# Kernel tuning notes

Hardware: AMD Instinct MI355X
Metric: run time of the kernel (lower is better)

## Reference

```python
import jax, jax.numpy as jnp
import numpy as np

D = 1024      # model dim
H = 16        # attention heads
E = 8         # experts
TOP_K = 2
CF = 1.25     # capacity factor
EPS = 1e-5
BAL_COEF = 1e-2
Z_COEF = 1e-3


def layer_norm(x, w, b):
    m = x.mean(-1, keepdims=True)
    var = ((x - m) ** 2).mean(-1, keepdims=True)
    return (x - m) * jax.lax.rsqrt(var + EPS) * w + b


def mha(q, k, v, in_w, in_b, out_w, out_b):
    B, S, d = q.shape
    dh = d // H
    wq, wk, wv = jnp.split(in_w, 3, axis=0)
    bq, bk, bv = jnp.split(in_b, 3)

    def proj(x, w, b):  # [B,S,d] -> [B,H,S,dh]
        return (x @ w.T + b).reshape(B, -1, H, dh).transpose(0, 2, 1, 3)

    qh, kh, vh = proj(q, wq, bq), proj(k, wk, bk), proj(v, wv, bv)
    scale = 1.0 / np.sqrt(dh)
    scores = jnp.einsum('bhqd,bhkd->bhqk', qh, kh) * scale
    attn = jax.nn.softmax(scores, axis=-1)
    o = jnp.einsum('bhqk,bhkd->bhqd', attn, vh).transpose(0, 2, 1, 3).reshape(B, S, d)
    return o @ out_w.T + out_b


def moe(x, router_w, w1, b1, w2, b2):
    B, S, d = x.shape
    t = x.reshape(-1, d)           # [N,d] tokens
    N = t.shape[0]
    C = int(np.ceil(TOP_K * N / E * CF))  # per-expert capacity (static)
    logits = t @ router_w          # [N,E]
    probs = jax.nn.softmax(logits, axis=-1)
    gates, idx = jax.lax.top_k(probs, TOP_K)   # [N,2]
    oh = jax.nn.one_hot(idx, E, dtype=t.dtype) # [N,2,E]
    m0, m1 = oh[:, 0], oh[:, 1]
    # position in expert buffer; first choices take priority over second
    pos0 = jnp.cumsum(m0, axis=0) - 1.0
    pos1 = jnp.cumsum(m1, axis=0) - 1.0 + m0.sum(axis=0, keepdims=True)
    v0 = m0 * (pos0 < C)
    v1 = m1 * (pos1 < C)
    p0 = jax.nn.one_hot(pos0.astype(jnp.int32), C, dtype=t.dtype) * v0[..., None]  # [N,E,C]
    p1 = jax.nn.one_hot(pos1.astype(jnp.int32), C, dtype=t.dtype) * v1[..., None]
    dispatch = p0 + p1
    combine = p0 * gates[:, 0, None, None] + p1 * gates[:, 1, None, None]
    # dispatch -> grouped GEMM -> combine
    xin = jnp.einsum('nec,nd->ecd', dispatch, t)                     # [E,C,d]
    h = jax.nn.gelu(jnp.einsum('ecd,edf->ecf', xin, w1) + b1[:, None, :])
    out_e = jnp.einsum('ecf,efd->ecd', h, w2) + b2[:, None, :]       # [E,C,d]
    y = jnp.einsum('nec,ecd->nd', combine, out_e).reshape(B, S, d)
    # aux losses: load-balance + router z-loss
    f = m0.mean(axis=0)            # fraction routed (top-1)
    P = probs.mean(axis=0)         # mean router prob
    balance = E * jnp.sum(f * P)
    zloss = jnp.mean(jax.nn.logsumexp(logits, axis=-1) ** 2)
    aux = BAL_COEF * balance + Z_COEF * zloss
    return y, aux


def setup_inputs() -> dict:
    key = jax.random.key(0)
    ks = jax.random.split(key, 16)
    s = 0.02
    Dff = 4 * D
    return {
        'q': jax.random.normal(ks[0], (8, 512, D), jnp.float32),
        'k': jax.random.normal(ks[1], (8, 512, D), jnp.float32),
        'v': jax.random.normal(ks[2], (8, 512, D), jnp.float32),
        'in_proj_w': jax.random.normal(ks[3], (3 * D, D), jnp.float32) * s,
        'in_proj_b': jnp.zeros((3 * D,), jnp.float32),
        'out_proj_w': jax.random.normal(ks[4], (D, D), jnp.float32) * s,
        'out_proj_b': jnp.zeros((D,), jnp.float32),
        'ln1_w': jnp.ones((D,), jnp.float32),
        'ln1_b': jnp.zeros((D,), jnp.float32),
        'ln2_w': jnp.ones((D,), jnp.float32),
        'ln2_b': jnp.zeros((D,), jnp.float32),
        'router_w': jax.random.normal(ks[5], (D, E), jnp.float32) * s,
        'w1': jax.random.normal(ks[6], (E, D, Dff), jnp.float32) * s,
        'b1': jnp.zeros((E, Dff), jnp.float32),
        'w2': jax.random.normal(ks[7], (E, Dff, D), jnp.float32) * s,
        'b2': jnp.zeros((E, D), jnp.float32),
    }


def reference(q, k, v, in_proj_w, in_proj_b, out_proj_w, out_proj_b,
              ln1_w, ln1_b, ln2_w, ln2_b, router_w, w1, b1, w2, b2):
    attn = mha(q, k, v, in_proj_w, in_proj_b, out_proj_w, out_proj_b)
    x = layer_norm(q + attn, ln1_w, ln1_b)
    y, aux = moe(x, router_w, w1, b1, w2, b2)
    x = layer_norm(x + y, ln2_w, ln2_b)
    return x, aux
```

## Files before the change

kernel.cpp:

```cpp
#include <hip/hip_runtime.h>
#include <cstdint>
#include <cstddef>

#define KB   8
#define KS   512
#define KD   1024
#define KH   16
#define KDH  64
#define KE   8
#define KDFF 4096
#define KN   4096
#define KCAP 1280
#define KCHB 32
#define KNCH 4
#define KPLE ((long)KN*KD)

typedef unsigned short u16;
typedef _Float16 f16;
typedef f16   f16x8 __attribute__((ext_vector_type(8)));
typedef float f32x4 __attribute__((ext_vector_type(4)));

#define RSCALE 4096.0f
#define RINV   2.44140625e-4f

__device__ __forceinline__ u16 f2h(float f){
  f16 h = (f16)f;
  return __builtin_bit_cast(u16, h);
}
__device__ __forceinline__ float h2f(u16 u){
  f16 h = __builtin_bit_cast(f16, u);
  return (float)h;
}
__device__ __forceinline__ void split2v(float f, u16 &a, u16 &b){
  f16 h0 = (f16)f;
  float r = (f - (float)h0) * RSCALE;
  a = __builtin_bit_cast(u16, h0);
  b = f2h(r);
}
__device__ __forceinline__ f16x8 ld8h(const u16* p){
  uint4 v = *(const uint4*)p;
  return __builtin_bit_cast(f16x8, v);
}
__device__ __forceinline__ void async16(const u16* g, u16* l){
  __builtin_amdgcn_global_load_lds(
      (const __attribute__((address_space(1))) unsigned int*)(g),
      (__attribute__((address_space(3))) unsigned int*)(l),
      16, 0, 0);
}

__device__ __forceinline__ int xcd_remap(int lin, int nwg){
  int qq = nwg >> 3, r8 = nwg & 7;
  int xcd = lin & 7, pos = lin >> 3;
  return (xcd < r8 ? xcd*(qq+1) : r8*(qq+1) + (xcd-r8)*qq) + pos;
}

struct GArgs {
  const u16 *A0, *A1;
  const u16 *B0, *B1;
  long lda, sA, ldb, sB;
  const float* bias; long biasStride;
  float* outF;
  u16 *o0;
  u16 *o1;
  int K, mode;
  int hbase;
  float scale;
};

template<int NP>
__launch_bounds__(256)
__global__ void gemm128(GArgs g){
  __shared__ __align__(16) u16 sm[NP*2*4096];
  const int tid  = threadIdx.x;
  const int lane = tid & 63;
  const int wave = tid >> 6;
  const int quad = lane >> 4;
  const int r    = lane & 15;
  const int wm = (wave & 1) * 64;
  const int wn = (wave >> 1) * 64;
  const int gx = gridDim.x, gy = gridDim.y;
  const int nwg = gx*gy*(int)gridDim.z;
  int lin = (int)blockIdx.x + gx*((int)blockIdx.y + gy*(int)blockIdx.z);
  lin = xcd_remap(lin, nwg);
  const int bx = lin % gx;
  const int byy = (lin / gx) % gy;
  const int z  = lin / (gx*gy);
  const long m0 = (long)byy * 128;
  const long n0 = (long)bx * 128;
  const u16* Ap[NP]; const u16* Bp[NP];
  if (g.mode == 2){
    int bh = g.hbase + z;
    long off = ((long)(bh >> 4)*KS)*KD + (long)(bh & 15)*KDH;
    Ap[0] = g.A0 + off; Bp[0] = g.B0 + off;
    if (NP == 2){ Ap[1] = g.A1 + off; Bp[1] = g.B1 + off; }
  } else {
    Ap[0] = g.A0 + (long)z*g.sA; Bp[0] = g.B0 + (long)z*g.sB;
    if (NP == 2){ Ap[1] = g.A1 + (long)z*g.sA; Bp[1] = g.B1 + (long)z*g.sB; }
  }
  const int srow   = tid >> 2;
  const int schunk = (tid & 3) ^ ((tid >> 3) & 3);
  f32x4 acc[4][4] = {};
  f32x4 accr[4][4] = {};
  for (int kt = 0; kt < g.K; kt += 32){
#pragma unroll
    for (int p = 0; p < NP; ++p){
#pragma unroll
      for (int r0 = 0; r0 < 2; ++r0){
        long row = r0*64 + srow;
        async16(Ap[p] + (m0 + row)*g.lda + kt + schunk*8, &sm[p*4096      + r0*2048 + wave*512]);
        async16(Bp[p] + (n0 + row)*g.ldb + kt + schunk*8, &sm[(NP+p)*4096 + r0*2048 + wave*512]);
      }
    }
    __syncthreads();
    f16x8 af[NP][4], bf[NP][4];
#pragma unroll
    for (int i = 0; i < 4; ++i){
      int row = wm + i*16 + r;
      int slot = quad ^ ((row >> 1) & 3);
#pragma unroll
      for (int p = 0; p < NP; ++p)
        af[p][i] = ld8h(&sm[p*4096 + row*32 + slot*8]);
    }
#pragma unroll
    for (int j = 0; j < 4; ++j){
      int row = wn + j*16 + r;
      int slot = quad ^ ((row >> 1) & 3);
#pragma unroll
      for (int p = 0; p < NP; ++p)
        bf[p][j] = ld8h(&sm[(NP+p)*4096 + row*32 + slot*8]);
    }
#pragma unroll
    for (int i = 0; i < 4; ++i)
#pragma unroll
      for (int j = 0; j < 4; ++j){
        acc[i][j] = __builtin_amdgcn_mfma_f32_16x16x32_f16(af[0][i], bf[0][j], acc[i][j], 0, 0, 0);
        if (NP == 2){
          accr[i][j] = __builtin_amdgcn_mfma_f32_16x16x32_f16(af[0][i], bf[1][j], accr[i][j], 0, 0, 0);
          accr[i][j] = __builtin_amdgcn_mfma_f32_16x16x32_f16(af[1][i], bf[0][j], accr[i][j], 0, 0, 0);
        }
      }
    __syncthreads();
  }
#pragma unroll
  for (int i = 0; i < 4; ++i){
#pragma unroll
    for (int rr = 0; rr < 4; ++rr){
      long row = m0 + wm + i*16 + quad*4 + rr;
#pragma unroll
      for (int j = 0; j < 4; ++j){
        long col = n0 + wn + j*16 + r;
        float v = acc[i][j][rr];
        if (NP == 2) v += accr[i][j][rr] * RINV;
        switch (g.mode){
          case 2: {
            g.outF[((long)z*KS + row)*KS + col] = v * g.scale;
            break;
          }
          case 4: {
            v += g.bias[col];
            g.outF[row*KD + col] = v;
            break;
          }
          case 5: {
            v += g.bias[(long)z*g.biasStride + col];
            float u = v + 0.044715f*v*v*v;
            v = 0.5f*v*(1.0f + tanhf(0.7978845608028654f*u));
            g.o0[((long)z*KCAP + row)*KDFF + col] = f2h(v);
            break;
          }
          case 6: {
            v += g.bias[(long)z*g.biasStride + col];
            g.o0[((long)z*KCAP + row)*KD + col] = f2h(v);
            break;
          }
          default: {
            v += g.bias[(long)z*g.biasStride + col];
            u16* d0 = (z < 2) ? (g.o0 + (long)z*2*KPLE) : g.o1;
            u16* d1 = d0 + KPLE;
            long idx = row*KD + col;
            unsigned short x, y; split2v(v, x, y);
            d0[idx] = x; d1[idx] = y;
            break;
          }
        }
      }
    }
  }
}

__launch_bounds__(256)
__global__ void gemm_pv(const u16* __restrict__ Ph, const u16* __restrict__ Pl,
                        const u16* __restrict__ V0, const u16* __restrict__ V1,
                        u16* __restrict__ O0, u16* __restrict__ O1, int chunkBase){
  __shared__ __align__(16) u16 sm[2*4096 + 2*2048];
  const int tid  = threadIdx.x;
  const int lane = tid & 63;
  const int wave = tid >> 6;
  const int quad = lane >> 4;
  const int r    = lane & 15;
  const int wm = (wave & 1) * 64;
  const int wn = (wave >> 1) * 32;
  const int gx = gridDim.x;
  const int nwg = gx*(int)gridDim.y;
  int lin = (int)blockIdx.x + gx*(int)blockIdx.y;
  lin = xcd_remap(lin, nwg);
  const int z  = lin / gx;
  const long m0 = (long)(lin % gx) * 128;
  const u16* Ap[2] = { Ph + (long)z*KS*KS,  Pl + (long)z*KS*KS };
  const u16* Bp[2] = { V0 + (long)z*KDH*KS, V1 + (long)z*KDH*KS };
  const int srow   = tid >> 2;
  const int schunk = (tid & 3) ^ ((tid >> 3) & 3);
  f32x4 acc[4][2] = {};
  f32x4 accr[4][2] = {};
  for (int kt = 0; kt < KS; kt += 32){
#pragma unroll
    for (int p = 0; p < 2; ++p){
#pragma unroll
      for (int r0 = 0; r0 < 2; ++r0){
        long row = r0*64 + srow;
        async16(Ap[p] + (m0 + row)*KS + kt + schunk*8, &sm[p*4096 + r0*2048 + wave*512]);
      }
      async16(Bp[p] + srow*KS + kt + schunk*8, &sm[8192 + p*2048 + wave*512]);
    }
    __syncthreads();
    f16x8 af[2][4], bf[2][2];
#pragma unroll
    for (int i = 0; i < 4; ++i){
      int row = wm + i*16 + r;
      int slot = quad ^ ((row >> 1) & 3);
#pragma unroll
      for (int p = 0; p < 2; ++p)
        af[p][i] = ld8h(&sm[p*4096 + row*32 + slot*8]);
    }
#pragma unroll
    for (int j = 0; j < 2; ++j){
      int row = wn + j*16 + r;
      int slot = quad ^ ((row >> 1) & 3);
#pragma unroll
      for (int p = 0; p < 2; ++p)
        bf[p][j] = ld8h(&sm[8192 + p*2048 + row*32 + slot*8]);
    }
#pragma unroll
    for (int i = 0; i < 4; ++i)
#pragma unroll
      for (int j = 0; j < 2; ++j){
        acc[i][j]  = __builtin_amdgcn_mfma_f32_16x16x32_f16(af[0][i], bf[0][j], acc[i][j], 0, 0, 0);
        accr[i][j] = __builtin_amdgcn_mfma_f32_16x16x32_f16(af[0][i], bf[1][j], accr[i][j], 0, 0, 0);
        accr[i][j] = __builtin_amdgcn_mfma_f32_16x16x32_f16(af[1][i], bf[0][j], accr[i][j], 0, 0, 0);
      }
    __syncthreads();
  }
  int bh = chunkBase + z;
  long b = bh >> 4, h = bh & 15;
#pragma unroll
  for (int i = 0; i < 4; ++i){
#pragma unroll
    for (int rr = 0; rr < 4; ++rr){
      long s = m0 + wm + i*16 + quad*4 + rr;
#pragma unroll
      for (int j = 0; j < 2; ++j){
        long col = wn + j*16 + r;
        float v = acc[i][j][rr] + accr[i][j][rr] * RINV;
        long idx = (b*KS + s)*KD + h*KDH + col;
        unsigned short x, y; split2v(v, x, y);
        O0[idx] = x; O1[idx] = y;
      }
    }
  }
}

__global__ void split2k(const float* __restrict__ x, u16* __restrict__ h,
                        u16* __restrict__ l, long n4){
  long i = (long)blockIdx.x*blockDim.x + threadIdx.x;
  if (i >= n4) return;
  float4 v = ((const float4*)x)[i];
  ushort4 a, b;
  split2v(v.x, a.x, b.x);
  split2v(v.y, a.y, b.y);
  split2v(v.z, a.z, b.z);
  split2v(v.w, a.w, b.w);
  ((ushort4*)h)[i] = a; ((ushort4*)l)[i] = b;
}

__global__ void trans_b(const float* __restrict__ in, u16* __restrict__ outp, int R, int Cc){
  __shared__ float tile[32][33];
  long z = blockIdx.z;
  const float* ip = in + z*(long)R*Cc;
  u16* op = outp + z*(long)R*Cc;
  int c0 = blockIdx.x*32, r0 = blockIdx.y*32;
  int tx = threadIdx.x, ty = threadIdx.y;
  for (int rr = ty; rr < 32; rr += 8)
    tile[rr][tx] = ip[(long)(r0+rr)*Cc + c0 + tx];
  __syncthreads();
  for (int cc = ty; cc < 32; cc += 8)
    op[(long)(c0+cc)*R + r0 + tx] = f2h(tile[tx][cc]);
}

__global__ void vtrans(const u16* __restrict__ in0, const u16* __restrict__ in1,
                       u16* __restrict__ out0, u16* __restrict__ out1){
  __shared__ u16 tile[2][32][33];
  int sT = blockIdx.x;
  int dT = blockIdx.y;
  int b  = blockIdx.z;
  int tx = threadIdx.x;
  int ty = threadIdx.y;
  long srow = (long)b*KS + sT*32;
  int d0 = dT*32;
  for (int rr = ty; rr < 32; rr += 8){
    tile[0][rr][tx] = in0[(srow+rr)*KD + d0 + tx];
    tile[1][rr][tx] = in1[(srow+rr)*KD + d0 + tx];
  }
  __syncthreads();
  int h = d0 >> 6;
  int dbase = d0 & 63;
  long obase = ((long)(b*KH + h)*KDH)*KS + sT*32 + tx;
  for (int cc = ty; cc < 32; cc += 8){
    long o = obase + (long)(dbase+cc)*KS;
    out0[o] = tile[0][tx][cc];
    out1[o] = tile[1][tx][cc];
  }
}

__launch_bounds__(64)
__global__ void softmax2(const float* __restrict__ scores, u16* __restrict__ ph,
                         u16* __restrict__ pl){
  long row = blockIdx.x;
  const float* rp = scores + row * KS;
  int lane = threadIdx.x;
  float4 a = ((const float4*)rp)[lane*2];
  float4 b = ((const float4*)rp)[lane*2 + 1];
  float vv[8] = {a.x,a.y,a.z,a.w,b.x,b.y,b.z,b.w};
  float m = vv[0];
#pragma unroll
  for (int t = 1; t < 8; ++t) m = fmaxf(m, vv[t]);
  for (int off = 32; off; off >>= 1) m = fmaxf(m, __shfl_xor(m, off));
  float s = 0.f;
#pragma unroll
  for (int t = 0; t < 8; ++t){ vv[t] = expf(vv[t] - m); s += vv[t]; }
  for (int off = 32; off; off >>= 1) s += __shfl_xor(s, off);
  float inv = 1.0f / s;
  unsigned short hh[8], ll[8];
#pragma unroll
  for (int t = 0; t < 8; ++t) split2v(vv[t] * inv, hh[t], ll[t]);
  ushort4* dh = (ushort4*)(ph + row*KS + lane*8);
  dh[0] = make_ushort4(hh[0],hh[1],hh[2],hh[3]);
  dh[1] = make_ushort4(hh[4],hh[5],hh[6],hh[7]);
  ushort4* dl = (ushort4*)(pl + row*KS + lane*8);
  dl[0] = make_ushort4(ll[0],ll[1],ll[2],ll[3]);
  dl[1] = make_ushort4(ll[4],ll[5],ll[6],ll[7]);
}

__launch_bounds__(256)
__global__ void ln1_router(const float* __restrict__ q, const float* __restrict__ attn,
    const float* __restrict__ lnw, const float* __restrict__ lnb, const float* __restrict__ rw,
    float* __restrict__ x1, u16* __restrict__ x1b,
    int* __restrict__ idx0, int* __restrict__ idx1, float* __restrict__ gate0, float* __restrict__ gate1,
    float* __restrict__ ptok, float* __restrict__ lset){
  const int t = blockIdx.x, tid = threadIdx.x;
  const int lane = tid & 63, wid = tid >> 6;
  float4 xv = ((const float4*)(q    + (long)t*KD))[tid];
  float4 av = ((const float4*)(attn + (long)t*KD))[tid];
  xv.x += av.x; xv.y += av.y; xv.z += av.z; xv.w += av.w;
  float s  = xv.x + xv.y + xv.z + xv.w;
  float ss = xv.x*xv.x + xv.y*xv.y + xv.z*xv.z + xv.w*xv.w;
  for (int off = 32; off; off >>= 1){ s += __shfl_xor(s, off); ss += __shfl_xor(ss, off); }
  __shared__ float rs[4], rss[4];
  if (lane == 0){ rs[wid] = s; rss[wid] = ss; }
  __syncthreads();
  float S1 = rs[0]+rs[1]+rs[2]+rs[3];
  float S2 = rss[0]+rss[1]+rss[2]+rss[3];
  float mean = S1 * (1.0f/KD);
  float var  = S2 * (1.0f/KD) - mean*mean;
  float rstd = rsqrtf(var + 1e-5f);
  float4 w4 = ((const float4*)lnw)[tid];
  float4 b4 = ((const float4*)lnb)[tid];
  float y0 = (xv.x - mean)*rstd*w4.x + b4.x;
  float y1 = (xv.y - mean)*rstd*w4.y + b4.y;
  float y2 = (xv.z - mean)*rstd*w4.z + b4.z;
  float y3 = (xv.w - mean)*rstd*w4.w + b4.w;
  float4 yo; yo.x=y0; yo.y=y1; yo.z=y2; yo.w=y3;
  ((float4*)(x1 + (long)t*KD))[tid] = yo;
  ushort4 yb; yb.x=f2h(y0); yb.y=f2h(y1); yb.z=f2h(y2); yb.w=f2h(y3);
  ((ushort4*)(x1b + (long)t*KD))[tid] = yb;
  int d0 = tid*4;
  float rloc[4][8];
#pragma unroll
  for (int c = 0; c < 4; ++c){
    const float4* rp = (const float4*)(rw + (long)(d0 + c)*KE);
    float4 u = rp[0], v2 = rp[1];
    rloc[c][0]=u.x; rloc[c][1]=u.y; rloc[c][2]=u.z; rloc[c][3]=u.w;
    rloc[c][4]=v2.x; rloc[c][5]=v2.y; rloc[c][6]=v2.z; rloc[c][7]=v2.w;
  }
  float yv[4] = {y0,y1,y2,y3};
  float pr[8];
#pragma unroll
  for (int e = 0; e < 8; ++e)
    pr[e] = yv[0]*rloc[0][e] + yv[1]*rloc[1][e] + yv[2]*rloc[2][e] + yv[3]*rloc[3][e];
#pragma unroll
  for (int e = 0; e < 8; ++e)
    for (int off = 32; off; off >>= 1) pr[e] += __shfl_xor(pr[e], off);
  __shared__ float wl[4][8];
  if (lane == 0)
#pragma unroll
    for (int e = 0; e < 8; ++e) wl[wid][e] = pr[e];
  __syncthreads();
  if (tid == 0){
    float lg[8];
#pragma unroll
    for (int e = 0; e < 8; ++e) lg[e] = wl[0][e]+wl[1][e]+wl[2][e]+wl[3][e];
    float mx = lg[0];
    for (int e = 1; e < 8; ++e) mx = fmaxf(mx, lg[e]);
    float pe[8], se = 0.f;
    for (int e = 0; e < 8; ++e){ pe[e] = expf(lg[e]-mx); se += pe[e]; }
    float inv = 1.0f/se;
    for (int e = 0; e < 8; ++e) pe[e] *= inv;
    int e0 = 0;
    for (int e = 1; e < 8; ++e) if (pe[e] > pe[e0]) e0 = e;
    int e1 = (e0 == 0) ? 1 : 0;
    for (int e = 0; e < 8; ++e) if (e != e0 && pe[e] > pe[e1]) e1 = e;
    idx0[t] = e0; idx1[t] = e1;
    gate0[t] = pe[e0]; gate1[t] = pe[e1];
    for (int e = 0; e < 8; ++e) ptok[(long)t*8 + e] = pe[e];
    lset[t] = mx + logf(se);
  }
}

__launch_bounds__(64)
__global__ void scan1(const int* __restrict__ idx0, const int* __restrict__ idx1,
                      int* __restrict__ rnk0, int* __restrict__ rnk1,
                      int* __restrict__ h0, int* __restrict__ h1){
  int lane = threadIdx.x;
  int t = blockIdx.x*64 + lane;
  int i0 = idx0[t], i1 = idx1[t];
  unsigned long long below = (1ull << lane) - 1ull;
  unsigned long long b0[8], b1[8];
#pragma unroll
  for (int e = 0; e < 8; ++e){
    b0[e] = __ballot(i0 == e);
    b1[e] = __ballot(i1 == e);
  }
  rnk0[t] = __popcll(b0[i0] & below);
  rnk1[t] = __popcll(b1[i1] & below);
  if (lane < 8){
    h0[blockIdx.x*8 + lane] = __popcll(b0[lane]);
    h1[blockIdx.x*8 + lane] = __popcll(b1[lane]);
  }
}

__launch_bounds__(64)
__global__ void scan2(const int* __restrict__ h0, const int* __restrict__ h1,
                      int* __restrict__ bs0, int* __restrict__ bs1, int* __restrict__ cnt0){
  int lane = threadIdx.x;
  for (int e = 0; e < 8; ++e){
    int v = h0[lane*8 + e];
    int x = v;
    for (int off = 1; off < 64; off <<= 1){
      int y = __shfl_up(x, off);
      if (lane >= off) x += y;
    }
    bs0[lane*8 + e] = x - v;
    int tot = __shfl(x, 63);
    if (lane == 0) cnt0[e] = tot;
    int w = h1[lane*8 + e];
    int xx = w;
    for (int off = 1; off < 64; off <<= 1){
      int y = __shfl_up(xx, off);
      if (lane >= off) xx += y;
    }
    bs1[lane*8 + e] = tot + xx - w;
  }
}

__global__ void scan3(const int* __restrict__ idx0, const int* __restrict__ idx1,
                      const int* __restrict__ rnk0, const int* __restrict__ rnk1,
                      const int* __restrict__ bs0, const int* __restrict__ bs1,
                      int* __restrict__ dst0, int* __restrict__ dst1, int* __restrict__ slot){
  int t = blockIdx.x*blockDim.x + threadIdx.x;
  if (t >= KN) return;
  int c = t >> 6;
  int e0 = idx0[t], e1 = idx1[t];
  int p0 = bs0[c*8 + e0] + rnk0[t];
  int p1 = bs1[c*8 + e1] + rnk1[t];
  int d0 = (p0 < KCAP) ? (e0*KCAP + p0) : -1;
  int d1 = (p1 < KCAP) ? (e1*KCAP + p1) : -1;
  dst0[t] = d0; dst1[t] = d1;
  if (d0 >= 0) slot[d0] = t;
  if (d1 >= 0) slot[d1] = t;
}

__launch_bounds__(64)
__global__ void gather_xin(const int* __restrict__ slot_token, const u16* __restrict__ x1b,
                           u16* __restrict__ xin){
  long slot = blockIdx.x;
  int t = slot_token[slot];
  uint4* dst = (uint4*)(xin + slot*KD);
  int lane = threadIdx.x;
  if (t >= 0){
    const uint4* src = (const uint4*)(x1b + (long)t*KD);
    dst[lane*2]   = src[lane*2];
    dst[lane*2+1] = src[lane*2+1];
  } else {
    uint4 zz; zz.x = zz.y = zz.z = zz.w = 0;
    dst[lane*2] = zz; dst[lane*2+1] = zz;
  }
}

__launch_bounds__(256)
__global__ void combine_ln2(const float* __restrict__ x1, const u16* __restrict__ oute,
    const int* __restrict__ dest0, const int* __restrict__ dest1,
    const float* __restrict__ gate0, const float* __restrict__ gate1,
    const float* __restrict__ lnw, const float* __restrict__ lnb, float* __restrict__ out){
  const int t = blockIdx.x, tid = threadIdx.x;
  const int lane = tid & 63, wid = tid >> 6;
  float4 xv = ((const float4*)(x1 + (long)t*KD))[tid];
  int d0 = dest0[t], d1 = dest1[t];
  float g0 = gate0[t], g1 = gate1[t];
  if (d0 >= 0){
    ushort4 o = ((const ushort4*)(oute + (long)d0*KD))[tid];
    xv.x += g0*h2f(o.x); xv.y += g0*h2f(o.y); xv.z += g0*h2f(o.z); xv.w += g0*h2f(o.w);
  }
  if (d1 >= 0){
    ushort4 o = ((const ushort4*)(oute + (long)d1*KD))[tid];
    xv.x += g1*h2f(o.x); xv.y += g1*h2f(o.y); xv.z += g1*h2f(o.z); xv.w += g1*h2f(o.w);
  }
  float s  = xv.x + xv.y + xv.z + xv.w;
  float ss = xv.x*xv.x + xv.y*xv.y + xv.z*xv.z + xv.w*xv.w;
  for (int off = 32; off; off >>= 1){ s += __shfl_xor(s, off); ss += __shfl_xor(ss, off); }
  __shared__ float rs[4], rss[4];
  if (lane == 0){ rs[wid] = s; rss[wid] = ss; }
  __syncthreads();
  float S1 = rs[0]+rs[1]+rs[2]+rs[3];
  float S2 = rss[0]+rss[1]+rss[2]+rss[3];
  float mean = S1 * (1.0f/KD);
  float var  = S2 * (1.0f/KD) - mean*mean;
  float rstd = rsqrtf(var + 1e-5f);
  float4 w4 = ((const float4*)lnw)[tid];
  float4 b4 = ((const float4*)lnb)[tid];
  float4 yo;
  yo.x = (xv.x - mean)*rstd*w4.x + b4.x;
  yo.y = (xv.y - mean)*rstd*w4.y + b4.y;
  yo.z = (xv.z - mean)*rstd*w4.z + b4.z;
  yo.w = (xv.w - mean)*rstd*w4.w + b4.w;
  ((float4*)(out + (long)t*KD))[tid] = yo;
}

__launch_bounds__(1024)
__global__ void aux_k(const int* __restrict__ cnt0, const float* __restrict__ ptok,
                      const float* __restrict__ lset, float* __restrict__ out){
  int t = threadIdx.x;
  float ps[8] = {0,0,0,0,0,0,0,0};
  float l2 = 0.f;
  for (int i = t; i < KN; i += 1024){
    const float4* p = (const float4*)(ptok + (long)i*8);
    float4 a = p[0], b = p[1];
    ps[0]+=a.x; ps[1]+=a.y; ps[2]+=a.z; ps[3]+=a.w;
    ps[4]+=b.x; ps[5]+=b.y; ps[6]+=b.z; ps[7]+=b.w;
    float l = lset[i]; l2 = fmaf(l, l, l2);
  }
#pragma unroll
  for (int off = 32; off; off >>= 1){
#pragma unroll
    for (int e = 0; e < 8; ++e) ps[e] += __shfl_xor(ps[e], off);
    l2 += __shfl_xor(l2, off);
  }
  __shared__ float sp[16][9];
  int lane = t & 63, wid = t >> 6;
  if (lane == 0){
#pragma unroll
    for (int e = 0; e < 8; ++e) sp[wid][e] = ps[e];
    sp[wid][8] = l2;
  }
  __syncthreads();
  if (t == 0){
    float fin[9];
#pragma unroll
    for (int j = 0; j < 9; ++j){
      float s = 0.f;
      for (int w2 = 0; w2 < 16; ++w2) s += sp[w2][j];
      fin[j] = s;
    }
    float bal = 0.f;
    for (int e = 0; e < 8; ++e)
      bal += ((float)cnt0[e] * (1.0f/KN)) * (fin[e] * (1.0f/KN));
    bal *= (float)KE;
    float zl = fin[8] * (1.0f/KN);
    out[(long)KN*KD] = 0.01f*bal + 0.001f*zl;
  }
}

extern "C" void kernel_launch(void* const* d_in, const int* in_sizes, int n_in,
                              void* d_out, int out_size, void* d_ws, size_t ws_size,
                              hipStream_t stream){
  const float* q    = (const float*)d_in[0];
  const float* k    = (const float*)d_in[1];
  const float* v    = (const float*)d_in[2];
  const float* inw  = (const float*)d_in[3];
  const float* inb  = (const float*)d_in[4];
  const float* outw = (const float*)d_in[5];
  const float* outb = (const float*)d_in[6];
  const float* ln1w = (const float*)d_in[7];
  const float* ln1b = (const float*)d_in[8];
  const float* ln2w = (const float*)d_in[9];
  const float* ln2b = (const float*)d_in[10];
  const float* rw   = (const float*)d_in[11];
  const float* w1   = (const float*)d_in[12];
  const float* b1   = (const float*)d_in[13];
  const float* w2   = (const float*)d_in[14];
  const float* b2   = (const float*)d_in[15];
  float* out = (float*)d_out;
  char* ws = (char*)d_ws;

  constexpr size_t PLB  = (size_t)KN*KD*2;
  constexpr long   PLE  = (long)KN*KD;
  constexpr size_t oW1T = 0;
  constexpr size_t oW2T = oW1T + 67108864;
  constexpr size_t oWQ0 = oW2T + 67108864;
  constexpr size_t oWQ1 = oWQ0 + 6291456;
  constexpr size_t oWO0 = oWQ1 + 6291456;
  constexpr size_t oWO1 = oWO0 + 2097152;
  constexpr size_t oX1  = oWO1 + 2097152;
  constexpr size_t oX1B = oX1  + 16777216;
  constexpr size_t oMISC= oX1B + 8388608;
  constexpr size_t oU1  = oMISC + 1048576;
  constexpr size_t oU2  = oU1 + 83886080;
  constexpr size_t oU3  = oU2 + 50331648;
  constexpr size_t oEND = oU3 + 67108864;
  if (ws_size < oEND) return;

  u16* W1T = (u16*)(ws + oW1T);
  u16* W2T = (u16*)(ws + oW2T);
  u16* WQ0 = (u16*)(ws + oWQ0); u16* WQ1 = (u16*)(ws + oWQ1);
  u16* WO0 = (u16*)(ws + oWO0); u16* WO1 = (u16*)(ws + oWO1);
  float* X1 = (float*)(ws + oX1);
  u16* X1B  = (u16*)(ws + oX1B);

  int*   IDX0 = (int*)(ws + oMISC);
  int*   IDX1 = (int*)(ws + oMISC + 16384);
  int*   RNK0 = (int*)(ws + oMISC + 32768);
  int*   RNK1 = (int*)(ws + oMISC + 49152);
  int*   DST0 = (int*)(ws + oMISC + 65536);
  int*   DST1 = (int*)(ws + oMISC + 81920);
  float* G0   = (float*)(ws + oMISC + 98304);
  float* G1   = (float*)(ws + oMISC + 114688);
  int*   H0   = (int*)(ws + oMISC + 131072);
  int*   H1   = (int*)(ws + oMISC + 133120);
  int*   BS0  = (int*)(ws + oMISC + 135168);
  int*   BS1  = (int*)(ws + oMISC + 137216);
  int*   CNT0 = (int*)(ws + oMISC + 139264);
  int*   SLOT = (int*)(ws + oMISC + 139776);
  float* PTOK = (float*)(ws + oMISC + 262144);
  float* LSET = (float*)(ws + oMISC + 393216);

  u16* Qs0 = (u16*)(ws + oU1);           u16* Qs1 = (u16*)(ws + oU1 + PLB);
  u16* Ks0 = (u16*)(ws + oU1 + 2*PLB);   u16* Ks1 = (u16*)(ws + oU1 + 3*PLB);
  u16* Vs0 = (u16*)(ws + oU1 + 4*PLB);   u16* Vs1 = (u16*)(ws + oU1 + 5*PLB);
  u16* VTOK0 = (u16*)(ws + oU1 + 6*PLB); u16* VTOK1 = (u16*)(ws + oU1 + 7*PLB);
  float* ATTN = (float*)(ws + oU1);
  u16* O0 = (u16*)(ws + oU1 + 16777216);
  u16* O1 = (u16*)(ws + oU1 + 16777216 + PLB);
  u16* HBUF = (u16*)(ws + oU1);

  u16* QT0 = (u16*)(ws + oU2);           u16* QT1 = (u16*)(ws + oU2 + PLB);
  u16* KT0 = (u16*)(ws + oU2 + 2*PLB);   u16* KT1 = (u16*)(ws + oU2 + 3*PLB);
  u16* VT0 = (u16*)(ws + oU2 + 4*PLB);   u16* VT1 = (u16*)(ws + oU2 + 5*PLB);
  u16* XIN  = (u16*)(ws + oU2);
  u16* OUTE = (u16*)(ws + oU2 + 20971520);

  float* SCF = (float*)(ws + oU3);
  u16* PH  = (u16*)(ws + oU3 + 33554432);
  u16* PL  = (u16*)(ws + oU3 + 50331648);

  hipMemsetAsync(ws + oMISC + 139776, 0xFF, (size_t)KE*KCAP*4, stream);

  split2k<<<4096, 256, 0, stream>>>(q, Qs0, Qs1, (long)KN*KD/4);
  split2k<<<4096, 256, 0, stream>>>(k, Ks0, Ks1, (long)KN*KD/4);
  split2k<<<4096, 256, 0, stream>>>(v, Vs0, Vs1, (long)KN*KD/4);
  split2k<<<3072, 256, 0, stream>>>(inw, WQ0, WQ1, 786432);
  split2k<<<1024, 256, 0, stream>>>(outw, WO0, WO1, 262144);

  trans_b<<<dim3(KDFF/32, KD/32, KE), dim3(32,8), 0, stream>>>(w1, W1T, KD, KDFF);
  trans_b<<<dim3(KD/32, KDFF/32, KE), dim3(32,8), 0, stream>>>(w2, W2T, KDFF, KD);

  {
    GArgs ga{};
    ga.A0=Qs0; ga.A1=Qs1; ga.lda=KD; ga.sA=2*PLE;
    ga.B0=WQ0; ga.B1=WQ1; ga.ldb=KD; ga.sB=1048576;
    ga.bias=inb; ga.biasStride=KD;
    ga.o0=QT0; ga.o1=VTOK0; ga.outF=nullptr;
    ga.K=KD; ga.mode=7; ga.scale=1.f;
    gemm128<2><<<dim3(8, 32, 3), 256, 0, stream>>>(ga);
  }

  vtrans<<<dim3(KS/32, KD/32, KB), dim3(32,8), 0, stream>>>(VTOK0, VTOK1, VT0, VT1);

  for (int c = 0; c < KNCH; ++c){
    long hoff = (long)c * KCHB * KS * KDH;
    GArgs gs{};
    gs.A0=QT0; gs.A1=QT1; gs.lda=KD; gs.sA=0;
    gs.B0=KT0; gs.B1=KT1; gs.ldb=KD; gs.sB=0;
    gs.hbase = c*KCHB;
    gs.bias=nullptr; gs.biasStride=0; gs.outF=SCF; gs.o0=nullptr;
    gs.K=KDH; gs.mode=2; gs.scale=0.125f;
    gemm128<2><<<dim3(4, 4, KCHB), 256, 0, stream>>>(gs);

    softmax2<<<KCHB*KS, 64, 0, stream>>>(SCF, PH, PL);

    gemm_pv<<<dim3(4, KCHB), 256, 0, stream>>>(PH, PL, VT0+hoff, VT1+hoff,
                                               O0, O1, c*KCHB);
  }

  {
    GArgs go{};
    go.A0=O0; go.A1=O1; go.lda=KD; go.sA=0;
    go.B0=WO0; go.B1=WO1; go.ldb=KD; go.sB=0;
    go.bias=outb; go.biasStride=0; go.outF=ATTN; go.o0=nullptr;
    go.K=KD; go.mode=4; go.scale=1.f;
    gemm128<2><<<dim3(8, 32, 1), 256, 0, stream>>>(go);
  }

  ln1_router<<<KN, 256, 0, stream>>>(q, ATTN, ln1w, ln1b, rw, X1, X1B,
                                     IDX0, IDX1, G0, G1, PTOK, LSET);
  scan1<<<64, 64, 0, stream>>>(IDX0, IDX1, RNK0, RNK1, H0, H1);
  scan2<<<1, 64, 0, stream>>>(H0, H1, BS0, BS1, CNT0);
  scan3<<<16, 256, 0, stream>>>(IDX0, IDX1, RNK0, RNK1, BS0, BS1, DST0, DST1, SLOT);
  aux_k<<<1, 1024, 0, stream>>>(CNT0, PTOK, LSET, out);
  gather_xin<<<KE*KCAP, 64, 0, stream>>>(SLOT, X1B, XIN);

  {
    GArgs f1{};
    f1.A0=XIN; f1.A1=nullptr; f1.lda=KD; f1.sA=(long)KCAP*KD;
    f1.B0=W1T; f1.B1=nullptr; f1.ldb=KD; f1.sB=(long)KDFF*KD;
    f1.bias=b1; f1.biasStride=KDFF; f1.outF=nullptr; f1.o0=HBUF;
    f1.K=KD; f1.mode=5; f1.scale=1.f;
    gemm128<1><<<dim3(KDFF/128, KCAP/128, KE), 256, 0, stream>>>(f1);

    GArgs f2{};
    f2.A0=HBUF; f2.A1=nullptr; f2.lda=KDFF; f2.sA=(long)KCAP*KDFF;
    f2.B0=W2T; f2.B1=nullptr; f2.ldb=KDFF; f2.sB=(long)KD*KDFF;
    f2.bias=b2; f2.biasStride=KD; f2.outF=nullptr; f2.o0=OUTE;
    f2.K=KDFF; f2.mode=6; f2.scale=1.f;
    gemm128<1><<<dim3(KD/128, KCAP/128, KE), 256, 0, stream>>>(f2);
  }

  combine_ln2<<<KN, 256, 0, stream>>>(X1, OUTE, DST0, DST1, G0, G1, ln2w, ln2b, out);
}
```

Measured before the change: 1.279 ms.

## Double-buffer LDS tiles in gemm128 and gemm_pv to overlap loads with MFMA

Both GEMM kernels now use two LDS buffers. The next K-tile's async global-to-LDS copies are issued before the MFMA work on the current tile, with one barrier per step. This is meant to hide global load latency behind compute instead of waiting on every tile. It doubles LDS use per block, which may lower occupancy, and it assumes K is an even multiple of 32 with at least two tiles.

```diff
diff --git a/kernel.cpp b/kernel.cpp
--- a/kernel.cpp
+++ b/kernel.cpp
@@ -70,7 +70,8 @@
 template<int NP>
 __launch_bounds__(256)
 __global__ void gemm128(GArgs g){
-  __shared__ __align__(16) u16 sm[NP*2*4096];
+  constexpr int BUF = NP*2*4096;
+  __shared__ __align__(16) u16 sm[2*BUF];
   const int tid  = threadIdx.x;
   const int lane = tid & 63;
   const int wave = tid >> 6;
@@ -101,17 +102,19 @@
   const int schunk = (tid & 3) ^ ((tid >> 3) & 3);
   f32x4 acc[4][4] = {};
   f32x4 accr[4][4] = {};
-  for (int kt = 0; kt < g.K; kt += 32){
+
+  auto STAGE = [&](int buf, int kt){
 #pragma unroll
     for (int p = 0; p < NP; ++p){
 #pragma unroll
       for (int r0 = 0; r0 < 2; ++r0){
         long row = r0*64 + srow;
-        async16(Ap[p] + (m0 + row)*g.lda + kt + schunk*8, &sm[p*4096      + r0*2048 + wave*512]);
-        async16(Bp[p] + (n0 + row)*g.ldb + kt + schunk*8, &sm[(NP+p)*4096 + r0*2048 + wave*512]);
+        async16(Ap[p] + (m0 + row)*g.lda + kt + schunk*8, &sm[buf + p*4096      + r0*2048 + wave*512]);
+        async16(Bp[p] + (n0 + row)*g.ldb + kt + schunk*8, &sm[buf + (NP+p)*4096 + r0*2048 + wave*512]);
       }
     }
-    __syncthreads();
+  };
+  auto COMPUTE = [&](int buf){
     f16x8 af[NP][4], bf[NP][4];
 #pragma unroll
     for (int i = 0; i < 4; ++i){
@@ -119,7 +122,7 @@
       int slot = quad ^ ((row >> 1) & 3);
 #pragma unroll
       for (int p = 0; p < NP; ++p)
-        af[p][i] = ld8h(&sm[p*4096 + row*32 + slot*8]);
+        af[p][i] = ld8h(&sm[buf + p*4096 + row*32 + slot*8]);
     }
 #pragma unroll
     for (int j = 0; j < 4; ++j){
@@ -127,7 +130,7 @@
       int slot = quad ^ ((row >> 1) & 3);
 #pragma unroll
       for (int p = 0; p < NP; ++p)
-        bf[p][j] = ld8h(&sm[(NP+p)*4096 + row*32 + slot*8]);
+        bf[p][j] = ld8h(&sm[buf + (NP+p)*4096 + row*32 + slot*8]);
     }
 #pragma unroll
     for (int i = 0; i < 4; ++i)
@@ -139,8 +142,24 @@
           accr[i][j] = __builtin_amdgcn_mfma_f32_16x16x32_f16(af[1][i], bf[0][j], accr[i][j], 0, 0, 0);
         }
       }
+  };
+
+  const int nk = g.K >> 5;
+  STAGE(0, 0);
+  __syncthreads();
+  for (int it = 0; it < nk - 2; it += 2){
+    STAGE(BUF, (it+1) << 5);
+    COMPUTE(0);
     __syncthreads();
-  }
+    STAGE(0, (it+2) << 5);
+    COMPUTE(BUF);
+    __syncthreads();
+  }
+  STAGE(BUF, (nk-1) << 5);
+  COMPUTE(0);
+  __syncthreads();
+  COMPUTE(BUF);
+
 #pragma unroll
   for (int i = 0; i < 4; ++i){
 #pragma unroll
@@ -192,7 +211,8 @@
 __global__ void gemm_pv(const u16* __restrict__ Ph, const u16* __restrict__ Pl,
                         const u16* __restrict__ V0, const u16* __restrict__ V1,
                         u16* __restrict__ O0, u16* __restrict__ O1, int chunkBase){
-  __shared__ __align__(16) u16 sm[2*4096 + 2*2048];
+  constexpr int BUF = 2*4096 + 2*2048;
+  __shared__ __align__(16) u16 sm[2*BUF];
   const int tid  = threadIdx.x;
   const int lane = tid & 63;
   const int wave = tid >> 6;
@@ -212,17 +232,19 @@
   const int schunk = (tid & 3) ^ ((tid >> 3) & 3);
   f32x4 acc[4][2] = {};
   f32x4 accr[4][2] = {};
-  for (int kt = 0; kt < KS; kt += 32){
+
+  auto STAGE = [&](int buf, int kt){
 #pragma unroll
     for (int p = 0; p < 2; ++p){
 #pragma unroll
       for (int r0 = 0; r0 < 2; ++r0){
         long row = r0*64 + srow;
-        async16(Ap[p] + (m0 + row)*KS + kt + schunk*8, &sm[p*4096 + r0*2048 + wave*512]);
+        async16(Ap[p] + (m0 + row)*KS + kt + schunk*8, &sm[buf + p*4096 + r0*2048 + wave*512]);
       }
-      async16(Bp[p] + srow*KS + kt + schunk*8, &sm[8192 + p*2048 + wave*512]);
-    }
-    __syncthreads();
+      async16(Bp[p] + srow*KS + kt + schunk*8, &sm[buf + 8192 + p*2048 + wave*512]);
+    }
+  };
+  auto COMPUTE = [&](int buf){
     f16x8 af[2][4], bf[2][2];
 #pragma unroll
     for (int i = 0; i < 4; ++i){
@@ -230,7 +252,7 @@
       int slot = quad ^ ((row >> 1) & 3);
 #pragma unroll
       for (int p = 0; p < 2; ++p)
-        af[p][i] = ld8h(&sm[p*4096 + row*32 + slot*8]);
+        af[p][i] = ld8h(&sm[buf + p*4096 + row*32 + slot*8]);
     }
 #pragma unroll
     for (int j = 0; j < 2; ++j){
@@ -238,7 +260,7 @@
       int slot = quad ^ ((row >> 1) & 3);
 #pragma unroll
       for (int p = 0; p < 2; ++p)
-        bf[p][j] = ld8h(&sm[8192 + p*2048 + row*32 + slot*8]);
+        bf[p][j] = ld8h(&sm[buf + 8192 + p*2048 + row*32 + slot*8]);
     }
 #pragma unroll
     for (int i = 0; i < 4; ++i)
@@ -248,8 +270,24 @@
         accr[i][j] = __builtin_amdgcn_mfma_f32_16x16x32_f16(af[0][i], bf[1][j], accr[i][j], 0, 0, 0);
         accr[i][j] = __builtin_amdgcn_mfma_f32_16x16x32_f16(af[1][i], bf[0][j], accr[i][j], 0, 0, 0);
       }
+  };
+
+  const int nk = KS >> 5;
+  STAGE(0, 0);
+  __syncthreads();
+  for (int it = 0; it < nk - 2; it += 2){
+    STAGE(BUF, (it+1) << 5);
+    COMPUTE(0);
     __syncthreads();
-  }
+    STAGE(0, (it+2) << 5);
+    COMPUTE(BUF);
+    __syncthreads();
+  }
+  STAGE(BUF, (nk-1) << 5);
+  COMPUTE(0);
+  __syncthreads();
+  COMPUTE(BUF);
+
   int bh = chunkBase + z;
   long b = bh >> 4, h = bh & 15;
 #pragma unroll
```

Result: faster. 1.214 ms (-5.1%).
